# Kernel tuning notes

Measured on AMD Instinct MI355X. Metric: run time of the kernel, lower is better.

## Reference

```python
import jax, jax.numpy as jnp
import numpy as np

B, T, N, F_IN = 8, 16, 1000, 16
E = 16000
H, D = 4, 32          # heads, gat_hidden_shape
HL = 64               # lstm hidden
OUT = 8
NEG_SLOPE = 0.2       # PyG GATConv default


def setup_inputs() -> dict:
    key = jax.random.key(0)
    ks = jax.random.split(key, 10)
    def init(k, shape, fan):
        return (jax.random.normal(k, shape, jnp.float32) / np.sqrt(fan)).astype(jnp.float32)
    x = jax.random.normal(ks[0], (B, T, N, F_IN), jnp.float32)
    edge_index = jax.random.randint(ks[1], (2, E), 0, N)
    W_gat = init(ks[2], (F_IN, H * D), F_IN)       # GATConv lin weight
    att_src = init(ks[3], (H, D), D)
    att_dst = init(ks[4], (H, D), D)
    b_gat = jnp.zeros((H * D,), jnp.float32)
    W_ih = init(ks[5], (4 * HL, H * D), H * D)     # LSTM, gate order i,f,g,o
    W_hh = init(ks[6], (4 * HL, HL), HL)
    b_ih = jnp.zeros((4 * HL,), jnp.float32)
    b_hh = jnp.zeros((4 * HL,), jnp.float32)
    W_clf = init(ks[7], (OUT, HL), HL)
    b_clf = jnp.zeros((OUT,), jnp.float32)
    return {"x": x, "edge_index": edge_index, "W_gat": W_gat, "att_src": att_src,
            "att_dst": att_dst, "b_gat": b_gat, "W_ih": W_ih, "W_hh": W_hh,
            "b_ih": b_ih, "b_hh": b_hh, "W_clf": W_clf, "b_clf": b_clf}


def reference(x, edge_index, W_gat, att_src, att_dst, b_gat,
              W_ih, W_hh, b_ih, b_hh, W_clf, b_clf):
    Bx, Tx, Nx, Fx = x.shape
    x_flat = x.reshape(Bx * Tx, Nx, Fx)
    # PyG GATConv adds self-loops by default
    loop = jnp.arange(Nx)
    src = jnp.concatenate([edge_index[0], loop])
    dst = jnp.concatenate([edge_index[1], loop])

    def gat_graph(xg):  # xg: [N, F]
        xp = (xg @ W_gat).reshape(Nx, H, D)                 # [N,H,D]
        a_s = jnp.einsum('nhd,hd->nh', xp, att_src)         # [N,H]
        a_d = jnp.einsum('nhd,hd->nh', xp, att_dst)
        e = jax.nn.leaky_relu(a_s[src] + a_d[dst], NEG_SLOPE)  # [E+N,H]
        m = jax.ops.segment_max(e, dst, num_segments=Nx)       # per-target softmax
        ex = jnp.exp(e - m[dst])
        denom = jax.ops.segment_sum(ex, dst, num_segments=Nx)
        alpha = ex / denom[dst]                                # [E+N,H]
        out = jax.ops.segment_sum(alpha[..., None] * xp[src], dst, num_segments=Nx)
        return out.reshape(Nx, H * D) + b_gat                  # [N, H*D]

    gat = jax.vmap(gat_graph)(x_flat)          # [B*T, N, H*D]
    gat = jax.nn.relu(gat)
    pooled = gat.max(axis=1)                   # global_max_pool -> [B*T, H*D]
    seq = pooled.reshape(Bx, Tx, H * D)

    h0 = jnp.zeros((Bx, HL), jnp.float32)
    c0 = jnp.zeros((Bx, HL), jnp.float32)

    def step(carry, xt):  # xt: [B, H*D]
        h, c = carry
        gates = xt @ W_ih.T + h @ W_hh.T + b_ih + b_hh
        i, f, g, o = jnp.split(gates, 4, axis=-1)
        i, f, o = jax.nn.sigmoid(i), jax.nn.sigmoid(f), jax.nn.sigmoid(o)
        g = jnp.tanh(g)
        c = f * c + i * g
        h = o * jnp.tanh(c)
        return (h, c), None

    (hT, _), _ = jax.lax.scan(step, (h0, c0), seq.transpose(1, 0, 2))
    return hT @ W_clf.T + b_clf                # [B, OUT]
```

## Files before the change

### kernel.cpp

```cpp
#include <hip/hip_runtime.h>
#include <hip/hip_bf16.h>
#include <stdint.h>

namespace {
constexpr int kB = 8, kT = 16, kN = 1000, kF = 16;
constexpr int kE = 16000;
constexpr int kH = 4, kHD = 128;
constexpr int kHL = 64, kOUT = 8;
constexpr int kG = kB * kT;
constexpr float kNeg = 0.2f;
constexpr int kPre = 1024;
constexpr int kNPW = 32;
constexpr int kBCAP = 64;

constexpr size_t CX_WG   = 0;
constexpr size_t CX_ATS  = CX_WG   + 2048;
constexpr size_t CX_ATD  = CX_ATS  + 128;
constexpr size_t CX_BG   = CX_ATD  + 128;
constexpr size_t CX_WIH  = CX_BG   + 128;
constexpr size_t CX_WHH  = CX_WIH  + 32768;
constexpr size_t CX_BIH  = CX_WHH  + 16384;
constexpr size_t CX_BHH  = CX_BIH  + 256;
constexpr size_t CX_WCLF = CX_BHH  + 256;
constexpr size_t CX_BCLF = CX_WCLF + 512;
constexpr size_t CX_TOTAL = CX_BCLF + 8;

constexpr size_t OFF_FLAG  = 0;
constexpr size_t OFF_ROW   = 256;
constexpr size_t OFF_COL   = 4352;
constexpr size_t OFF_POOL  = 68608;
constexpr size_t OFF_CANON = 134400;
constexpr size_t OFF_AS    = 239872;
constexpr size_t OFF_BUCKET = OFF_AS + (size_t)kG * 288000;
constexpr size_t BUCKET_BYTES = (size_t)kN * kBCAP * 4;
constexpr size_t OFF_PPART  = OFF_BUCKET + 256000;
constexpr size_t PART25_BYTES = (size_t)kG * 25 * kHD * 4;
constexpr size_t PART50_BYTES = (size_t)kG * 50 * kHD * 4;

constexpr int kSetupBlocks = 41;
}

typedef float v2f __attribute__((ext_vector_type(2)));

__device__ __forceinline__ float bf2f(unsigned short u) {
    return __uint_as_float(((uint32_t)u) << 16);
}
__device__ __forceinline__ float blo(uint32_t u) { return __uint_as_float(u << 16); }
__device__ __forceinline__ float bhi(uint32_t u) { return __uint_as_float(u & 0xffff0000u); }
__device__ __forceinline__ v2f bfx2(uint32_t u) {
    __hip_bfloat162 h = *reinterpret_cast<__hip_bfloat162*>(&u);
    const float2 f = __bfloat1622float2(h);
    return (v2f){f.x, f.y};
}
__device__ __forceinline__ unsigned short f2bf(float f) {
    uint32_t u = __float_as_uint(f);
    uint32_t r = (u + 0x7fff + ((u >> 16) & 1)) >> 16;
    return (unsigned short)r;
}
__device__ __forceinline__ float sigm(float x) { return 1.f / (1.f + __expf(-x)); }

__device__ __forceinline__ int detect_isf_wave(const unsigned short* xs, int lane) {
    const uint2 s4 = *(const uint2*)(xs + lane * 4);
    const unsigned short u0 = (unsigned short)(s4.x & 0xffff);
    const unsigned short u1 = (unsigned short)(s4.x >> 16);
    const unsigned short u2 = (unsigned short)(s4.y & 0xffff);
    const unsigned short u3 = (unsigned short)(s4.y >> 16);
    int loc = 0;
#define ISF_TEST(u) { int ex = ((u) >> 7) & 0xff; \
    loc += ((u) == 0 || (ex >= 97 && ex <= 143)) ? 1 : 0; }
    ISF_TEST(u0) ISF_TEST(u1) ISF_TEST(u2) ISF_TEST(u3)
#undef ISF_TEST
#pragma unroll
    for (int sft = 1; sft < 64; sft <<= 1) loc += __shfl_xor(loc, sft, 64);
    return (loc >= 205) ? 0 : 1;
}

struct ConvArgs {
    const unsigned short* src[10];
    int n[10];
};

__global__ __launch_bounds__(256) void mega_setup(
        const void* __restrict__ xraw, const int* __restrict__ ei,
        ConvArgs ca,
        const unsigned short* __restrict__ WgR,
        const unsigned short* __restrict__ atsR,
        const unsigned short* __restrict__ atdR,
        int* __restrict__ flag, int* __restrict__ rowdeg, int* __restrict__ col,
        int* __restrict__ bucket, int use_bucket,
        unsigned short* __restrict__ canon,
        unsigned short* __restrict__ xp_all,
        float* __restrict__ as_all, float* __restrict__ ad_all,
        unsigned int* __restrict__ pooled) {
    const int t = threadIdx.x;
    const unsigned short* xs = (const unsigned short*)xraw;

    if (blockIdx.x < 8) {
        const int isf = detect_isf_wave(xs, t & 63);
        if (blockIdx.x == 0 && t == 0) *flag = isf;
        const int gid = (int)blockIdx.x * 256 + t;
        size_t base = 0;
        for (int s = 0; s < 10; ++s) {
            const int n = ca.n[s];
            if (isf) {
                const float* fp = (const float*)ca.src[s];
                for (int i = gid; i < n; i += 2048) canon[base + i] = f2bf(fp[i]);
            } else {
                const unsigned short* sp = ca.src[s];
                for (int i = gid; i < n; i += 2048) canon[base + i] = sp[i];
            }
            base += (size_t)n;
        }
    } else if (blockIdx.x == 8) {
        for (int i = t; i < kG * kHD; i += 256) pooled[i] = 0u;
    } else if (blockIdx.x < kSetupBlocks) {
        if (use_bucket) {
            const int gid = (int)(blockIdx.x - 9) * 256 + t;
            const int* srcp = ei;
            const int* dstp = ei + kE;
            for (int e = gid; e < kE; e += 32 * 256) {
                const int d = dstp[e];
                const int pos = atomicAdd(&rowdeg[d], 1);
                if (pos < kBCAP) bucket[d * kBCAP + pos] = srcp[e];
            }
        } else if (blockIdx.x == 9) {
            __shared__ int cnt[1024];
            __shared__ int wtot[4];
            const int lane = t & 63, w = t >> 6;
            for (int i = t; i < 1024; i += 256) cnt[i] = 0;
            __syncthreads();
            const int* dst = ei + kE;
            for (int e = t; e < kE; e += 256) atomicAdd(&cnt[dst[e]], 1);
            __syncthreads();
            const int n0 = 4 * t;
            int c0 = cnt[n0], c1 = cnt[n0 + 1], c2 = cnt[n0 + 2], c3 = cnt[n0 + 3];
            int s0 = c0, s1 = s0 + c1, s2 = s1 + c2, s3 = s2 + c3;
            int tot = s3;
#pragma unroll
            for (int sft = 1; sft < 64; sft <<= 1) {
                int v = __shfl_up(tot, sft, 64);
                if (lane >= sft) tot += v;
            }
            if (lane == 63) wtot[w] = tot;
            __syncthreads();
            int wexcl = 0;
            for (int j = 0; j < w; ++j) wexcl += wtot[j];
            const int excl = wexcl + tot - s3;
            if (t == 0) rowdeg[0] = 0;
            if (n0 < kN) {
                rowdeg[n0 + 1] = excl + s0;
                rowdeg[n0 + 2] = excl + s1;
                rowdeg[n0 + 3] = excl + s2;
                rowdeg[n0 + 4] = excl + s3;
            }
            __syncthreads();
            cnt[n0] = excl; cnt[n0 + 1] = excl + s0;
            cnt[n0 + 2] = excl + s1; cnt[n0 + 3] = excl + s2;
            __syncthreads();
            for (int e = t; e < kE; e += 256) {
                int d0 = dst[e];
                int pos = atomicAdd(&cnt[d0], 1);
                col[pos] = ei[e];
            }
        }
    } else {
        const int lane = t & 63;
        const int isf = detect_isf_wave(xs, lane);
        const int wv = t >> 6;
        const int wid = (int)(blockIdx.x - kSetupBlocks) * 4 + wv;

        float wA[kF], wB[kF];
        float as0, as1, ad0, ad1;
        if (isf) {
            const float* wf = (const float*)WgR;
#pragma unroll
            for (int f = 0; f < kF; ++f) {
                const float2 wp = ((const float2*)(wf + (size_t)f * kHD))[lane];
                wA[f] = wp.x; wB[f] = wp.y;
            }
            const float2 sv = ((const float2*)atsR)[lane];
            as0 = sv.x; as1 = sv.y;
            const float2 dv2 = ((const float2*)atdR)[lane];
            ad0 = dv2.x; ad1 = dv2.y;
        } else {
            const uint32_t* w32 = (const uint32_t*)WgR;
#pragma unroll
            for (int f = 0; f < kF; ++f) {
                const uint32_t u = w32[f * 64 + lane];
                wA[f] = blo(u); wB[f] = bhi(u);
            }
            const uint32_t us = ((const uint32_t*)atsR)[lane];
            as0 = blo(us); as1 = bhi(us);
            const uint32_t ud = ((const uint32_t*)atdR)[lane];
            ad0 = blo(ud); ad1 = bhi(ud);
        }

        uint32_t* xp32 = (uint32_t*)xp_all;
        const int nStart = wid * kNPW;
        const int nEnd = min(nStart + kNPW, kG * kN);
        if (nStart >= nEnd) return;

        auto emit = [&](int node, const float* xv) {
            float vA = 0.f, vB = 0.f;
#pragma unroll
            for (int f = 0; f < kF; ++f) {
                vA = fmaf(xv[f], wA[f], vA);
                vB = fmaf(xv[f], wB[f], vB);
            }
            xp32[(size_t)node * 64 + lane] =
                (uint32_t)f2bf(vA) | ((uint32_t)f2bf(vB) << 16);
            float aS = vA * as0 + vB * as1;
            float aD = vA * ad0 + vB * ad1;
#pragma unroll
            for (int sft = 1; sft < 16; sft <<= 1) {
                aS += __shfl_xor(aS, sft, 64);
                aD += __shfl_xor(aD, sft, 64);
            }
            if ((lane & 15) == 0) {
                as_all[(size_t)node * kH + (lane >> 4)] = aS;
                ad_all[(size_t)node * kH + (lane >> 4)] = aD;
            }
        };

        if (isf) {
            const float4* xr = (const float4*)xraw;
            float4 c0 = xr[(size_t)nStart * 4 + 0], c1 = xr[(size_t)nStart * 4 + 1];
            float4 c2 = xr[(size_t)nStart * 4 + 2], c3 = xr[(size_t)nStart * 4 + 3];
            for (int node = nStart; node < nEnd; ++node) {
                const int nn = (node + 1 < nEnd) ? node + 1 : node;
                const float4 p0 = xr[(size_t)nn * 4 + 0];
                const float4 p1 = xr[(size_t)nn * 4 + 1];
                const float4 p2 = xr[(size_t)nn * 4 + 2];
                const float4 p3 = xr[(size_t)nn * 4 + 3];
                const float xv[kF] = {c0.x, c0.y, c0.z, c0.w, c1.x, c1.y, c1.z, c1.w,
                                      c2.x, c2.y, c2.z, c2.w, c3.x, c3.y, c3.z, c3.w};
                emit(node, xv);
                c0 = p0; c1 = p1; c2 = p2; c3 = p3;
            }
        } else {
            const uint4* xr = (const uint4*)xs;
            uint4 c0 = xr[(size_t)nStart * 2 + 0], c1 = xr[(size_t)nStart * 2 + 1];
            for (int node = nStart; node < nEnd; ++node) {
                const int nn = (node + 1 < nEnd) ? node + 1 : node;
                const uint4 p0 = xr[(size_t)nn * 2 + 0];
                const uint4 p1 = xr[(size_t)nn * 2 + 1];
                const v2f f0 = bfx2(c0.x), f1 = bfx2(c0.y);
                const v2f f2 = bfx2(c0.z), f3 = bfx2(c0.w);
                const v2f f4 = bfx2(c1.x), f5 = bfx2(c1.y);
                const v2f f6 = bfx2(c1.z), f7 = bfx2(c1.w);
                const float xv[kF] = {
                    f0.x, f0.y, f1.x, f1.y, f2.x, f2.y, f3.x, f3.y,
                    f4.x, f4.y, f5.x, f5.y, f6.x, f6.y, f7.x, f7.y};
                emit(node, xv);
                c0 = p0; c1 = p1;
            }
        }
    }
}

template <int NB>
__global__ __launch_bounds__(256) void gat_aggregate(
        const int* __restrict__ rowdeg, const int* __restrict__ col,
        const int* __restrict__ bucket, int use_bucket,
        const unsigned short* __restrict__ xp,
        const float* __restrict__ a_s, const float* __restrict__ a_d,
        const unsigned short* __restrict__ bg,
        unsigned int* __restrict__ pooled,
        float* __restrict__ part, int use_part) {
    constexpr int NPB = kN / NB;
    constexpr int ITERS = NPB / 4;

    __shared__ float2 colal[4][4][68];
    __shared__ float pm[4][kHD];

    const int w = threadIdx.x >> 6;
    const int lane = threadIdx.x & 63;
    const int sub = lane >> 4;
    const int cl = lane & 15;
    const int hh = cl >> 2;
    const int xcd = blockIdx.x & 7;
    const int j = blockIdx.x >> 3;
    const int gl = xcd + 8 * (j / NB);
    const int blk = j % NB;
    const size_t gn = (size_t)gl * kN;
    const char* xpcl = (const char*)(xp + gn * kHD) + cl * 16;
    const float4* as4 = (const float4*)a_s + gn;
    const float4* ad4 = (const float4*)a_d + gn;
    const uint32_t* bg32 = (const uint32_t*)bg;
    float bgv[8];
#pragma unroll
    for (int jb = 0; jb < 4; ++jb) {
        uint32_t u = bg32[cl * 4 + jb];
        bgv[2 * jb] = blo(u);
        bgv[2 * jb + 1] = bhi(u);
    }
    float pool[8];
#pragma unroll
    for (int jb = 0; jb < 8; ++jb) pool[jb] = 0.f;

    auto pairBody = [&](v2f* acc2, float& dh, int e0) {
        const float2 cA = colal[w][hh][e0 + sub];
        const float2 cB = colal[w][hh][e0 + 4 + sub];
        const uint4 uA = *(const uint4*)(xpcl + __float_as_int(cA.x));
        const uint4 uB = *(const uint4*)(xpcl + __float_as_int(cB.x));
        const float aA = cA.y, aB = cB.y;
        const v2f aA2 = {aA, aA}, aB2 = {aB, aB};
        acc2[0] += aA2 * bfx2(uA.x);
        acc2[1] += aA2 * bfx2(uA.y);
        acc2[2] += aA2 * bfx2(uA.z);
        acc2[3] += aA2 * bfx2(uA.w);
        acc2[0] += aB2 * bfx2(uB.x);
        acc2[1] += aB2 * bfx2(uB.y);
        acc2[2] += aB2 * bfx2(uB.z);
        acc2[3] += aB2 * bfx2(uB.w);
        dh += aA + aB;
    };
    auto singleBody = [&](v2f* acc2, float& dh, int e0) {
        const float2 cA = colal[w][hh][e0 + sub];
        const uint4 uA = *(const uint4*)(xpcl + __float_as_int(cA.x));
        const float aA = cA.y;
        const v2f aA2 = {aA, aA};
        acc2[0] += aA2 * bfx2(uA.x);
        acc2[1] += aA2 * bfx2(uA.y);
        acc2[2] += aA2 * bfx2(uA.z);
        acc2[3] += aA2 * bfx2(uA.w);
        dh += aA;
    };
    auto finishNode = [&](v2f* acc2, float dh) {
        float acc[8];
#pragma unroll
        for (int jb = 0; jb < 4; ++jb) {
            acc[2 * jb] = acc2[jb].x;
            acc[2 * jb + 1] = acc2[jb].y;
        }
#pragma unroll
        for (int jb = 0; jb < 8; ++jb) {
            acc[jb] += __shfl_xor(acc[jb], 16, 64);
            acc[jb] += __shfl_xor(acc[jb], 32, 64);
        }
        dh += __shfl_xor(dh, 16, 64);
        dh += __shfl_xor(dh, 32, 64);
        const float inv = 1.f / dh;
#pragma unroll
        for (int jb = 0; jb < 8; ++jb) {
            const float o = acc[jb] * inv + bgv[jb];
            pool[jb] = fmaxf(pool[jb], o > 0.f ? o : 0.f);
        }
    };

    if (use_bucket) {
        int n0i = blk * NPB + w;
        int degc = min(rowdeg[n0i], 63);
        int sc = (lane < degc) ? bucket[n0i * kBCAP + lane] : n0i;
        float4 avc = as4[sc];
        float4 dvc = ad4[n0i];

        for (int it = 0; it < ITERS; ++it) {
            const int deg = degc;
            const int E = deg + 1;
            const int cntP = (E + 3) & ~3;
            const int s = sc;
            const float4 av = avc;
            const float4 dv = dvc;

            if (lane < cntP) {
                float p0 = 0.f, p1 = 0.f, p2 = 0.f, p3 = 0.f;
                if (lane < E) {
                    float t0 = av.x + dv.x, t1 = av.y + dv.y;
                    float t2 = av.z + dv.z, t3 = av.w + dv.w;
                    t0 = t0 > 0.f ? t0 : kNeg * t0;
                    t1 = t1 > 0.f ? t1 : kNeg * t1;
                    t2 = t2 > 0.f ? t2 : kNeg * t2;
                    t3 = t3 > 0.f ? t3 : kNeg * t3;
                    p0 = __expf(t0); p1 = __expf(t1);
                    p2 = __expf(t2); p3 = __expf(t3);
                }
                const float cf = __int_as_float(s << 8);
                colal[w][0][lane] = make_float2(cf, p0);
                colal[w][1][lane] = make_float2(cf, p1);
                colal[w][2][lane] = make_float2(cf, p2);
                colal[w][3][lane] = make_float2(cf, p3);
            }

            const int itn = (it + 1 == ITERS) ? 0 : (it + 1);
            const int n_nxt = blk * NPB + itn * 4 + w;
            degc = min(rowdeg[n_nxt], 63);
            dvc = ad4[n_nxt];
            sc = (lane < degc) ? bucket[n_nxt * kBCAP + lane] : n_nxt;

            v2f acc2[4];
#pragma unroll
            for (int jb = 0; jb < 4; ++jb) acc2[jb] = (v2f){0.f, 0.f};
            float dh = 0.f;
            int e0 = 0;
            if (cntP >= 8) { pairBody(acc2, dh, 0); e0 = 8; }
            avc = as4[sc];
            for (; e0 + 8 <= cntP; e0 += 8) pairBody(acc2, dh, e0);
            if (e0 < cntP) singleBody(acc2, dh, e0);

            finishNode(acc2, dh);
        }
    } else {
        for (int it = 0; it < ITERS; ++it) {
            const int n = blk * NPB + it * 4 + w;
            const int r0 = rowdeg[n];
            const int deg = rowdeg[n + 1] - r0;
            const int E = deg + 1;
            const float4 dv = ad4[n];
            v2f acc2[4];
#pragma unroll
            for (int jb = 0; jb < 4; ++jb) acc2[jb] = (v2f){0.f, 0.f};
            float dh = 0.f;

            for (int base = 0; base < E; base += 64) {
                const int cnt = min(64, E - base);
                const int cntP = (cnt + 3) & ~3;
                if (lane < cntP) {
                    const int eg = base + lane;
                    const bool act = lane < cnt;
                    const int s = (act && eg < deg) ? col[r0 + eg] : n;
                    float p0 = 0.f, p1 = 0.f, p2 = 0.f, p3 = 0.f;
                    if (act) {
                        const float4 av = as4[s];
                        float t0 = av.x + dv.x, t1 = av.y + dv.y;
                        float t2 = av.z + dv.z, t3 = av.w + dv.w;
                        t0 = t0 > 0.f ? t0 : kNeg * t0;
                        t1 = t1 > 0.f ? t1 : kNeg * t1;
                        t2 = t2 > 0.f ? t2 : kNeg * t2;
                        t3 = t3 > 0.f ? t3 : kNeg * t3;
                        p0 = __expf(t0); p1 = __expf(t1);
                        p2 = __expf(t2); p3 = __expf(t3);
                    }
                    const float cf = __int_as_float(s << 8);
                    colal[w][0][lane] = make_float2(cf, p0);
                    colal[w][1][lane] = make_float2(cf, p1);
                    colal[w][2][lane] = make_float2(cf, p2);
                    colal[w][3][lane] = make_float2(cf, p3);
                }
                int e0 = 0;
                for (; e0 + 8 <= cntP; e0 += 8) pairBody(acc2, dh, e0);
                if (e0 < cntP) singleBody(acc2, dh, e0);
            }
            finishNode(acc2, dh);
        }
    }

    if (sub == 0) {
#pragma unroll
        for (int jb = 0; jb < 8; ++jb) pm[w][cl * 8 + jb] = pool[jb];
    }
    __syncthreads();
    if (w == 0 && sub == 0) {
        if (use_part) {
            float* dst = part + ((size_t)gl * NB + blk) * kHD;
#pragma unroll
            for (int jb = 0; jb < 8; ++jb) {
                const int c = cl * 8 + jb;
                dst[c] = fmaxf(fmaxf(pm[0][c], pm[1][c]), fmaxf(pm[2][c], pm[3][c]));
            }
        } else {
            const size_t gp = (size_t)gl * kHD;
#pragma unroll
            for (int jb = 0; jb < 8; ++jb) {
                const int c = cl * 8 + jb;
                float vmax = fmaxf(fmaxf(pm[0][c], pm[1][c]), fmaxf(pm[2][c], pm[3][c]));
                atomicMax(pooled + gp + c, __float_as_uint(vmax));
            }
        }
    }
}

template <int NB>
__global__ __launch_bounds__(256) void lstm_gates_x(
        const float* __restrict__ pooled, const float* __restrict__ part,
        int use_part,
        const unsigned short* __restrict__ Wih,
        const unsigned short* __restrict__ bih,
        const unsigned short* __restrict__ bhh,
        float* __restrict__ gx) {
    const int g = blockIdx.x;
    const int r = threadIdx.x;
    __shared__ float xt[kHD];

    if (r < kHD) {
        if (use_part) {
            const float* ps = part + (size_t)g * NB * kHD + r;
            float v = ps[0];
#pragma unroll
            for (int k = 1; k < NB; ++k) v = fmaxf(v, ps[(size_t)k * kHD]);
            xt[r] = v;
        } else {
            xt[r] = pooled[(size_t)g * kHD + r];
        }
    }
    __syncthreads();

    const uint32_t* pw = (const uint32_t*)(Wih + (size_t)r * kHD);
    float a0 = 0.f, a1 = 0.f, a2 = 0.f, a3 = 0.f;
#pragma unroll
    for (int j = 0; j < 64; j += 4) {
        const v2f f0 = bfx2(pw[j]),     f1 = bfx2(pw[j + 1]);
        const v2f f2 = bfx2(pw[j + 2]), f3 = bfx2(pw[j + 3]);
        a0 += f0.x * xt[2 * j + 0] + f0.y * xt[2 * j + 1];
        a1 += f1.x * xt[2 * j + 2] + f1.y * xt[2 * j + 3];
        a2 += f2.x * xt[2 * j + 4] + f2.y * xt[2 * j + 5];
        a3 += f3.x * xt[2 * j + 6] + f3.y * xt[2 * j + 7];
    }
    gx[(size_t)g * 256 + r] = bf2f(bih[r]) + bf2f(bhh[r]) + (a0 + a1) + (a2 + a3);
}

__global__ __launch_bounds__(256) void lstm_seq(
        const float* __restrict__ gx,
        const unsigned short* __restrict__ Whh,
        const unsigned short* __restrict__ Wclf,
        const unsigned short* __restrict__ bclf,
        const int* __restrict__ flag,
        void* __restrict__ out) {
    const int b = blockIdx.x;
    const int r = threadIdx.x;
    __shared__ float hs[kHL];
    __shared__ float gates[4 * kHL];

    uint32_t whh[32];
    const uint32_t* ph = (const uint32_t*)(Whh + (size_t)r * kHL);
#pragma unroll
    for (int j = 0; j < 32; ++j) whh[j] = ph[j];

    float c_st = 0.f;
    if (r < kHL) hs[r] = 0.f;
    __syncthreads();

    for (int t = 0; t < kT; ++t) {
        const float gxv = gx[((size_t)b * kT + t) * 256 + r];
        float a0 = 0.f, a1 = 0.f, a2 = 0.f, a3 = 0.f;
#pragma unroll
        for (int j = 0; j < 32; j += 4) {
            const v2f f0 = bfx2(whh[j]),     f1 = bfx2(whh[j + 1]);
            const v2f f2 = bfx2(whh[j + 2]), f3 = bfx2(whh[j + 3]);
            a0 += f0.x * hs[2 * j + 0] + f0.y * hs[2 * j + 1];
            a1 += f1.x * hs[2 * j + 2] + f1.y * hs[2 * j + 3];
            a2 += f2.x * hs[2 * j + 4] + f2.y * hs[2 * j + 5];
            a3 += f3.x * hs[2 * j + 6] + f3.y * hs[2 * j + 7];
        }
        gates[r] = gxv + (a0 + a1) + (a2 + a3);
        __syncthreads();
        if (r < kHL) {
            const float iv = sigm(gates[r]);
            const float fv = sigm(gates[kHL + r]);
            const float gv = tanhf(gates[2 * kHL + r]);
            const float ov = sigm(gates[3 * kHL + r]);
            c_st = fv * c_st + iv * gv;
            hs[r] = ov * tanhf(c_st);
        }
        __syncthreads();
    }
    if (r < kOUT) {
        float acc = bf2f(bclf[r]);
#pragma unroll
        for (int k = 0; k < kHL; ++k) acc += hs[k] * bf2f(Wclf[r * kHL + k]);
        if (*flag) ((float*)out)[b * kOUT + r] = acc;
        else ((__hip_bfloat16*)out)[b * kOUT + r] = __float2bfloat16(acc);
    }
}

extern "C" void kernel_launch(void* const* d_in, const int* in_sizes, int n_in,
                              void* d_out, int out_size, void* d_ws, size_t ws_size,
                              hipStream_t stream) {
    const int* ei = (const int*)d_in[1];

    char* ws = (char*)d_ws;
    int*            flag   = (int*)(ws + OFF_FLAG);
    int*            rowdeg = (int*)(ws + OFF_ROW);
    int*            colv   = (int*)(ws + OFF_COL);
    unsigned int*   pooled = (unsigned int*)(ws + OFF_POOL);
    unsigned short* canon  = (unsigned short*)(ws + OFF_CANON);

    unsigned short* cBg   = canon + CX_BG;
    unsigned short* cWih  = canon + CX_WIH;
    unsigned short* cWhh  = canon + CX_WHH;
    unsigned short* cBih  = canon + CX_BIH;
    unsigned short* cBhh  = canon + CX_BHH;
    unsigned short* cWclf = canon + CX_WCLF;
    unsigned short* cBclf = canon + CX_BCLF;

    float*          a_s = (float*)(ws + OFF_AS);
    float*          a_d = (float*)(ws + OFF_AS + (size_t)kG * 16000);
    unsigned short* xp  = (unsigned short*)(ws + OFF_AS + (size_t)kG * 32000);
    float*          gx  = (float*)(ws + OFF_AS);

    const int use_bucket = (ws_size >= OFF_PPART) ? 1 : 0;
    const int part50_ok  = (ws_size >= OFF_PPART + PART50_BYTES) ? 1 : 0;
    const int part25_ok  = (ws_size >= OFF_PPART + PART25_BYTES) ? 1 : 0;
    const int use_part   = (part50_ok || part25_ok) ? 1 : 0;
    int* bucket = (int*)(ws + OFF_BUCKET);
    float* part = (float*)(ws + OFF_PPART);

    ConvArgs ca;
    const int sizes[10] = {2048, 128, 128, 128, 32768, 16384, 256, 256, 512, 8};
    const int which[10] = {2, 3, 4, 5, 6, 7, 8, 9, 10, 11};
    for (int i = 0; i < 10; ++i) {
        ca.src[i] = (const unsigned short*)d_in[which[i]];
        ca.n[i] = sizes[i];
    }

    hipMemsetAsync(ws + OFF_ROW, 0, 4096, stream);

    mega_setup<<<kSetupBlocks + kPre, 256, 0, stream>>>(
        d_in[0], ei, ca,
        (const unsigned short*)d_in[2], (const unsigned short*)d_in[3],
        (const unsigned short*)d_in[4],
        flag, rowdeg, colv, bucket, use_bucket, canon, xp, a_s, a_d, pooled);
    if (part50_ok) {
        gat_aggregate<50><<<kG * 50, 256, 0, stream>>>(
            rowdeg, colv, bucket, use_bucket, xp, a_s, a_d, cBg,
            pooled, part, 1);
        lstm_gates_x<50><<<kG, 256, 0, stream>>>(
            (const float*)pooled, part, 1, cWih, cBih, cBhh, gx);
    } else {
        gat_aggregate<25><<<kG * 25, 256, 0, stream>>>(
            rowdeg, colv, bucket, use_bucket, xp, a_s, a_d, cBg,
            pooled, part, use_part);
        lstm_gates_x<25><<<kG, 256, 0, stream>>>(
            (const float*)pooled, part, use_part, cWih, cBih, cBhh, gx);
    }
    lstm_seq<<<kB, 256, 0, stream>>>(gx, cWhh, cWclf, cBclf, flag, d_out);
}
```

Before: 185.7 us.

## Process two target nodes per wave concurrently in GAT aggregation with 25 blocks per graph

Each wave now works on two destination nodes at once, with double-slot shared memory for the attention coefficients. The gathers of the two nodes are interleaved so more independent memory loads are in flight. The launch is fixed at 25 blocks per graph with 40 nodes each, dropping the 50-block variant that the large workspace selected before. This raises per-thread register pressure and halves the block count, which may reduce occupancy.

```diff
diff --git a/kernel.cpp b/kernel.cpp
--- a/kernel.cpp
+++ b/kernel.cpp
@@ -9,6 +9,9 @@
 constexpr int kHL = 64, kOUT = 8;
 constexpr int kG = kB * kT;
 constexpr float kNeg = 0.2f;
+constexpr int kNB = 25;
+constexpr int kNPB = 40;
+constexpr int kPAIRS = 5;
 constexpr int kPre = 1024;
 constexpr int kNPW = 32;
 constexpr int kBCAP = 64;
@@ -34,8 +37,7 @@
 constexpr size_t OFF_BUCKET = OFF_AS + (size_t)kG * 288000;
 constexpr size_t BUCKET_BYTES = (size_t)kN * kBCAP * 4;
 constexpr size_t OFF_PPART  = OFF_BUCKET + 256000;
-constexpr size_t PART25_BYTES = (size_t)kG * 25 * kHD * 4;
-constexpr size_t PART50_BYTES = (size_t)kG * 50 * kHD * 4;
+constexpr size_t PART_BYTES = (size_t)kG * kNB * kHD * 4;
 
 constexpr int kSetupBlocks = 41;
 }
@@ -258,7 +260,6 @@
     }
 }
 
-template <int NB>
 __global__ __launch_bounds__(256) void gat_aggregate(
         const int* __restrict__ rowdeg, const int* __restrict__ col,
         const int* __restrict__ bucket, int use_bucket,
@@ -267,10 +268,7 @@
         const unsigned short* __restrict__ bg,
         unsigned int* __restrict__ pooled,
         float* __restrict__ part, int use_part) {
-    constexpr int NPB = kN / NB;
-    constexpr int ITERS = NPB / 4;
-
-    __shared__ float2 colal[4][4][68];
+    __shared__ float2 colal[4][2][4][68];
     __shared__ float pm[4][kHD];
 
     const int w = threadIdx.x >> 6;
@@ -280,8 +278,8 @@
     const int hh = cl >> 2;
     const int xcd = blockIdx.x & 7;
     const int j = blockIdx.x >> 3;
-    const int gl = xcd + 8 * (j / NB);
-    const int blk = j % NB;
+    const int gl = xcd + 8 * (j / kNB);
+    const int blk = j % kNB;
     const size_t gn = (size_t)gl * kN;
     const char* xpcl = (const char*)(xp + gn * kHD) + cl * 16;
     const float4* as4 = (const float4*)a_s + gn;
@@ -298,9 +296,9 @@
 #pragma unroll
     for (int jb = 0; jb < 8; ++jb) pool[jb] = 0.f;
 
-    auto pairBody = [&](v2f* acc2, float& dh, int e0) {
-        const float2 cA = colal[w][hh][e0 + sub];
-        const float2 cB = colal[w][hh][e0 + 4 + sub];
+    auto gatherPair = [&](int slot, v2f* acc2, float& dh, int e0) {
+        const float2 cA = colal[w][slot][hh][e0 + sub];
+        const float2 cB = colal[w][slot][hh][e0 + 4 + sub];
         const uint4 uA = *(const uint4*)(xpcl + __float_as_int(cA.x));
         const uint4 uB = *(const uint4*)(xpcl + __float_as_int(cB.x));
         const float aA = cA.y, aB = cB.y;
@@ -315,8 +313,8 @@
         acc2[3] += aB2 * bfx2(uB.w);
         dh += aA + aB;
     };
-    auto singleBody = [&](v2f* acc2, float& dh, int e0) {
-        const float2 cA = colal[w][hh][e0 + sub];
+    auto gatherSingle = [&](int slot, v2f* acc2, float& dh, int e0) {
+        const float2 cA = colal[w][slot][hh][e0 + sub];
         const uint4 uA = *(const uint4*)(xpcl + __float_as_int(cA.x));
         const float aA = cA.y;
         const v2f aA2 = {aA, aA};
@@ -326,6 +324,26 @@
         acc2[3] += aA2 * bfx2(uA.w);
         dh += aA;
     };
+    auto phase1 = [&](int slot, int s, int E, int cntP, float4 av, float4 dv) {
+        if (lane < cntP) {
+            float p0 = 0.f, p1 = 0.f, p2 = 0.f, p3 = 0.f;
+            if (lane < E) {
+                float t0 = av.x + dv.x, t1 = av.y + dv.y;
+                float t2 = av.z + dv.z, t3 = av.w + dv.w;
+                t0 = t0 > 0.f ? t0 : kNeg * t0;
+                t1 = t1 > 0.f ? t1 : kNeg * t1;
+                t2 = t2 > 0.f ? t2 : kNeg * t2;
+                t3 = t3 > 0.f ? t3 : kNeg * t3;
+                p0 = __expf(t0); p1 = __expf(t1);
+                p2 = __expf(t2); p3 = __expf(t3);
+            }
+            const float cf = __int_as_float(s << 8);
+            colal[w][slot][0][lane] = make_float2(cf, p0);
+            colal[w][slot][1][lane] = make_float2(cf, p1);
+            colal[w][slot][2][lane] = make_float2(cf, p2);
+            colal[w][slot][3][lane] = make_float2(cf, p3);
+        }
+    };
     auto finishNode = [&](v2f* acc2, float dh) {
         float acc[8];
 #pragma unroll
@@ -349,60 +367,56 @@
     };
 
     if (use_bucket) {
-        int n0i = blk * NPB + w;
-        int degc = min(rowdeg[n0i], 63);
-        int sc = (lane < degc) ? bucket[n0i * kBCAP + lane] : n0i;
-        float4 avc = as4[sc];
-        float4 dvc = ad4[n0i];
-
-        for (int it = 0; it < ITERS; ++it) {
-            const int deg = degc;
-            const int E = deg + 1;
-            const int cntP = (E + 3) & ~3;
-            const int s = sc;
-            const float4 av = avc;
-            const float4 dv = dvc;
-
-            if (lane < cntP) {
-                float p0 = 0.f, p1 = 0.f, p2 = 0.f, p3 = 0.f;
-                if (lane < E) {
-                    float t0 = av.x + dv.x, t1 = av.y + dv.y;
-                    float t2 = av.z + dv.z, t3 = av.w + dv.w;
-                    t0 = t0 > 0.f ? t0 : kNeg * t0;
-                    t1 = t1 > 0.f ? t1 : kNeg * t1;
-                    t2 = t2 > 0.f ? t2 : kNeg * t2;
-                    t3 = t3 > 0.f ? t3 : kNeg * t3;
-                    p0 = __expf(t0); p1 = __expf(t1);
-                    p2 = __expf(t2); p3 = __expf(t3);
-                }
-                const float cf = __int_as_float(s << 8);
-                colal[w][0][lane] = make_float2(cf, p0);
-                colal[w][1][lane] = make_float2(cf, p1);
-                colal[w][2][lane] = make_float2(cf, p2);
-                colal[w][3][lane] = make_float2(cf, p3);
-            }
-
-            const int itn = (it + 1 == ITERS) ? 0 : (it + 1);
-            const int n_nxt = blk * NPB + itn * 4 + w;
-            degc = min(rowdeg[n_nxt], 63);
-            dvc = ad4[n_nxt];
-            sc = (lane < degc) ? bucket[n_nxt * kBCAP + lane] : n_nxt;
-
-            v2f acc2[4];
-#pragma unroll
-            for (int jb = 0; jb < 4; ++jb) acc2[jb] = (v2f){0.f, 0.f};
-            float dh = 0.f;
-            int e0 = 0;
-            if (cntP >= 8) { pairBody(acc2, dh, 0); e0 = 8; }
-            avc = as4[sc];
-            for (; e0 + 8 <= cntP; e0 += 8) pairBody(acc2, dh, e0);
-            if (e0 < cntP) singleBody(acc2, dh, e0);
-
-            finishNode(acc2, dh);
+        int nA = blk * kNPB + w, nB = nA + 4;
+        int degA = min(rowdeg[nA], 63), degB = min(rowdeg[nB], 63);
+        int sA = (lane < degA) ? bucket[nA * kBCAP + lane] : nA;
+        int sB = (lane < degB) ? bucket[nB * kBCAP + lane] : nB;
+        float4 avA = as4[sA], avB = as4[sB];
+        float4 dvA = ad4[nA], dvB = ad4[nB];
+
+        for (int p = 0; p < kPAIRS; ++p) {
+            const int EA = degA + 1, EB = degB + 1;
+            const int cAp = (EA + 3) & ~3, cBp = (EB + 3) & ~3;
+
+            phase1(0, sA, EA, cAp, avA, dvA);
+            phase1(1, sB, EB, cBp, avB, dvB);
+
+            const int pn = (p + 1 == kPAIRS) ? 0 : (p + 1);
+            const int nA2 = blk * kNPB + pn * 8 + w, nB2 = nA2 + 4;
+            const int degA2 = min(rowdeg[nA2], 63);
+            const int degB2 = min(rowdeg[nB2], 63);
+            const float4 dvA2 = ad4[nA2], dvB2 = ad4[nB2];
+            const int sA2 = (lane < degA2) ? bucket[nA2 * kBCAP + lane] : nA2;
+            const int sB2 = (lane < degB2) ? bucket[nB2 * kBCAP + lane] : nB2;
+
+            v2f accA[4], accB[4];
+#pragma unroll
+            for (int jb = 0; jb < 4; ++jb) {
+                accA[jb] = (v2f){0.f, 0.f};
+                accB[jb] = (v2f){0.f, 0.f};
+            }
+            float dhA = 0.f, dhB = 0.f;
+            int eA = 0, eB = 0;
+            if (cAp >= 8) { gatherPair(0, accA, dhA, 0); eA = 8; }
+            if (cBp >= 8) { gatherPair(1, accB, dhB, 0); eB = 8; }
+            const float4 avA2 = as4[sA2];
+            const float4 avB2 = as4[sB2];
+            while (eA + 8 <= cAp || eB + 8 <= cBp) {
+                if (eA + 8 <= cAp) { gatherPair(0, accA, dhA, eA); eA += 8; }
+                if (eB + 8 <= cBp) { gatherPair(1, accB, dhB, eB); eB += 8; }
+            }
+            if (eA < cAp) gatherSingle(0, accA, dhA, eA);
+            if (eB < cBp) gatherSingle(1, accB, dhB, eB);
+
+            finishNode(accA, dhA);
+            finishNode(accB, dhB);
+
+            degA = degA2; sA = sA2; avA = avA2; dvA = dvA2;
+            degB = degB2; sB = sB2; avB = avB2; dvB = dvB2;
         }
     } else {
-        for (int it = 0; it < ITERS; ++it) {
-            const int n = blk * NPB + it * 4 + w;
+        for (int it = 0; it < kNPB / 4; ++it) {
+            const int n = blk * kNPB + it * 4 + w;
             const int r0 = rowdeg[n];
             const int deg = rowdeg[n + 1] - r0;
             const int E = deg + 1;
@@ -432,14 +446,14 @@
                         p2 = __expf(t2); p3 = __expf(t3);
                     }
                     const float cf = __int_as_float(s << 8);
-                    colal[w][0][lane] = make_float2(cf, p0);
-                    colal[w][1][lane] = make_float2(cf, p1);
-                    colal[w][2][lane] = make_float2(cf, p2);
-                    colal[w][3][lane] = make_float2(cf, p3);
+                    colal[w][0][0][lane] = make_float2(cf, p0);
+                    colal[w][0][1][lane] = make_float2(cf, p1);
+                    colal[w][0][2][lane] = make_float2(cf, p2);
+                    colal[w][0][3][lane] = make_float2(cf, p3);
                 }
                 int e0 = 0;
-                for (; e0 + 8 <= cntP; e0 += 8) pairBody(acc2, dh, e0);
-                if (e0 < cntP) singleBody(acc2, dh, e0);
+                for (; e0 + 8 <= cntP; e0 += 8) gatherPair(0, acc2, dh, e0);
+                if (e0 < cntP) gatherSingle(0, acc2, dh, e0);
             }
             finishNode(acc2, dh);
         }
@@ -452,7 +466,7 @@
     __syncthreads();
     if (w == 0 && sub == 0) {
         if (use_part) {
-            float* dst = part + ((size_t)gl * NB + blk) * kHD;
+            float* dst = part + ((size_t)gl * kNB + blk) * kHD;
 #pragma unroll
             for (int jb = 0; jb < 8; ++jb) {
                 const int c = cl * 8 + jb;
@@ -470,7 +484,6 @@
     }
 }
 
-template <int NB>
 __global__ __launch_bounds__(256) void lstm_gates_x(
         const float* __restrict__ pooled, const float* __restrict__ part,
         int use_part,
@@ -484,10 +497,10 @@
 
     if (r < kHD) {
         if (use_part) {
-            const float* ps = part + (size_t)g * NB * kHD + r;
+            const float* ps = part + (size_t)g * kNB * kHD + r;
             float v = ps[0];
 #pragma unroll
-            for (int k = 1; k < NB; ++k) v = fmaxf(v, ps[(size_t)k * kHD]);
+            for (int k = 1; k < kNB; ++k) v = fmaxf(v, ps[(size_t)k * kHD]);
             xt[r] = v;
         } else {
             xt[r] = pooled[(size_t)g * kHD + r];
@@ -589,9 +602,7 @@
     float*          gx  = (float*)(ws + OFF_AS);
 
     const int use_bucket = (ws_size >= OFF_PPART) ? 1 : 0;
-    const int part50_ok  = (ws_size >= OFF_PPART + PART50_BYTES) ? 1 : 0;
-    const int part25_ok  = (ws_size >= OFF_PPART + PART25_BYTES) ? 1 : 0;
-    const int use_part   = (part50_ok || part25_ok) ? 1 : 0;
+    const int use_part   = (ws_size >= OFF_PPART + PART_BYTES) ? 1 : 0;
     int* bucket = (int*)(ws + OFF_BUCKET);
     float* part = (float*)(ws + OFF_PPART);
 
@@ -610,18 +621,10 @@
         (const unsigned short*)d_in[2], (const unsigned short*)d_in[3],
         (const unsigned short*)d_in[4],
         flag, rowdeg, colv, bucket, use_bucket, canon, xp, a_s, a_d, pooled);
-    if (part50_ok) {
-        gat_aggregate<50><<<kG * 50, 256, 0, stream>>>(
-            rowdeg, colv, bucket, use_bucket, xp, a_s, a_d, cBg,
-            pooled, part, 1);
-        lstm_gates_x<50><<<kG, 256, 0, stream>>>(
-            (const float*)pooled, part, 1, cWih, cBih, cBhh, gx);
-    } else {
-        gat_aggregate<25><<<kG * 25, 256, 0, stream>>>(
-            rowdeg, colv, bucket, use_bucket, xp, a_s, a_d, cBg,
-            pooled, part, use_part);
-        lstm_gates_x<25><<<kG, 256, 0, stream>>>(
-            (const float*)pooled, part, use_part, cWih, cBih, cBhh, gx);
-    }
+    gat_aggregate<<<kG * kNB, 256, 0, stream>>>(rowdeg, colv, bucket, use_bucket,
+                                                xp, a_s, a_d, cBg,
+                                                pooled, part, use_part);
+    lstm_gates_x<<<kG, 256, 0, stream>>>((const float*)pooled, part, use_part,
+                                         cWih, cBih, cBhh, gx);
     lstm_seq<<<kB, 256, 0, stream>>>(gx, cWhh, cWclf, cBclf, flag, d_out);
 }
```

After: 192.4 us. 3.6% more time.
